# Performance work log

Hardware: AMD Instinct MI355X
Metric: run time of the kernel (lower is better)

The kernel has to match this reference:

```python
import jax, jax.numpy as jnp
import numpy as np

B, T, F, H, O = 64, 2048, 128, 512, 4
G = 4 * H  # gates: i, f, g, o (PyTorch order)


def setup_inputs() -> dict:
    key = jax.random.key(0)
    ks = jax.random.split(key, 12)
    s = 1.0 / np.sqrt(H)  # PyTorch LSTM init scale
    return {
        "x": jax.random.normal(ks[0], (B, T, F), dtype=jnp.float32),
        "W_ih_l0": jax.random.uniform(ks[1], (G, F), jnp.float32, -s, s),
        "W_hh_l0": jax.random.uniform(ks[2], (G, H), jnp.float32, -s, s),
        "b_ih_l0": jax.random.uniform(ks[3], (G,), jnp.float32, -s, s),
        "b_hh_l0": jax.random.uniform(ks[4], (G,), jnp.float32, -s, s),
        "W_ih_l1": jax.random.uniform(ks[5], (G, H), jnp.float32, -s, s),
        "W_hh_l1": jax.random.uniform(ks[6], (G, H), jnp.float32, -s, s),
        "b_ih_l1": jax.random.uniform(ks[7], (G,), jnp.float32, -s, s),
        "b_hh_l1": jax.random.uniform(ks[8], (G,), jnp.float32, -s, s),
        "W_out": jax.random.uniform(ks[9], (O, H), jnp.float32, -s, s),
        "b_out": jax.random.uniform(ks[10], (O,), jnp.float32, -s, s),
    }


def lstm_layer(x_seq, W_ih, W_hh, b_ih, b_hh):
    # x_seq: [B, T, Fin] -> (h_seq [B, T, H], h_final [B, H])
    b = x_seq.shape[0]
    h_dim = W_hh.shape[1]
    # Precompute input projections for all timesteps in one big GEMM.
    x_proj = jnp.einsum('btf,gf->btg', x_seq, W_ih) + b_ih + b_hh  # [B, T, 4H]

    def step(carry, xp_t):
        h, c = carry
        gates = xp_t + h @ W_hh.T  # [B, 4H]
        i, f, g, o = jnp.split(gates, 4, axis=-1)
        i = jax.nn.sigmoid(i)
        f = jax.nn.sigmoid(f)
        g = jnp.tanh(g)
        o = jax.nn.sigmoid(o)
        c = f * c + i * g
        h = o * jnp.tanh(c)
        return (h, c), h

    h0 = jnp.zeros((b, h_dim), x_seq.dtype)
    c0 = jnp.zeros((b, h_dim), x_seq.dtype)
    (hT, _), hs = jax.lax.scan(step, (h0, c0), jnp.swapaxes(x_proj, 0, 1))
    return jnp.swapaxes(hs, 0, 1), hT


def reference(x, W_ih_l0, W_hh_l0, b_ih_l0, b_hh_l0,
              W_ih_l1, W_hh_l1, b_ih_l1, b_hh_l1, W_out, b_out):
    h0_seq, h0_final = lstm_layer(x, W_ih_l0, W_hh_l0, b_ih_l0, b_hh_l0)
    _, h1_final = lstm_layer(h0_seq, W_ih_l1, W_hh_l1, b_ih_l1, b_hh_l1)
    # hn = stack([h0_final, h1_final]); relu(hn); linear applied to hn[0]
    hn0 = jax.nn.relu(h0_final)  # [B, H]
    out = hn0 @ W_out.T + b_out  # [B, 4]
    return out
```

## Files before the change

### kernel.cpp

```cpp
#include <hip/hip_runtime.h>
#include <hip/hip_bf16.h>
#include <cstdint>
#include <cstddef>


#define B_ 64
#define T_ 2048
#define F_ 128
#define H_ 512

#define NBLK 128
#define NTHR 256

#define ACT_STRIDE 1280
#define SMEM_SZ (16 * ACT_STRIDE)
#define HSLOT (B_ * H_)

typedef __bf16 bf16;
typedef __bf16 bf16x4 __attribute__((ext_vector_type(4)));
typedef __bf16 bf16x8 __attribute__((ext_vector_type(8)));
typedef float f32x4 __attribute__((ext_vector_type(4)));
typedef unsigned int u32;
typedef u32 u32x2 __attribute__((ext_vector_type(2)));
typedef u32 u32x4 __attribute__((ext_vector_type(4)));

static __device__ __forceinline__ float sigm(float v) {
  return 1.f / (1.f + __expf(-v));
}
static __device__ __forceinline__ float tanh_f(float v) {
  float a = fminf(fabsf(v), 20.f);
  float e = __expf(-2.f * a);
  float t = 1.f - 2.f * e / (1.f + e);
  return copysignf(t, v);
}
static __device__ __forceinline__ u32 bf16bits(float f) {
  bf16 b = (bf16)f;
  unsigned short us;
  __builtin_memcpy(&us, &b, 2);
  return (u32)us;
}

__global__ void __launch_bounds__(NTHR) prep_kernel(u32* hbuf) {
  int idx = blockIdx.x * blockDim.x + threadIdx.x;
  hbuf[idx] = 0u;
}

__global__ void __launch_bounds__(NTHR) xconv_kernel(
    const float* __restrict__ x, bf16* __restrict__ xbf) {
  const int b = blockIdx.x;
  const int t0 = blockIdx.y * 256;
  const int f2 = threadIdx.x & 63;
  const int tq = threadIdx.x >> 6;
  const int rg = b >> 4, row = b & 15;
  for (int i = 0; i < 64; ++i) {
    int t = t0 + i * 4 + tq;
    float2 xv = *(const float2*)(x + ((size_t)b * T_ + t) * F_ + 2 * f2);
    u32 w = bf16bits(xv.x) | (bf16bits(xv.y) << 16);
    *(u32*)((char*)xbf + ((((size_t)t * 4 + rg) * 16 + row) * 128 + 2 * f2) * 2) = w;
  }
}

__global__ void __launch_bounds__(NTHR, 1) lstm_kernel(
    const float* __restrict__ x,
    const float* __restrict__ Wih,
    const float* __restrict__ Whh,
    const float* __restrict__ bih,
    const float* __restrict__ bhh,
    u32* __restrict__ hbuf,
    float* __restrict__ hf32,
    const bf16* __restrict__ xbf)
{
  __shared__ __align__(16) char smem[SMEM_SZ];

  const int tid = threadIdx.x;
  const int bid = blockIdx.x;
  const int rg = bid >> 5;
  const int jg = bid & 31;
  const int row0 = rg * 16;
  const int j0 = jg * 16;

  const int lane = tid & 63;
  const int wave = tid >> 6;
  const int fr = lane & 15;
  const int kg = lane >> 4;

  bf16x8 wfrag[20];
  {
    const int G = (fr >> 2) * H_ + j0 + wave * 4 + (fr & 3);
    const float* sih = Wih + (size_t)G * F_;
    const float* shh = Whh + (size_t)G * H_;
    #pragma unroll
    for (int kk = 0; kk < 20; ++kk) {
      const float* s = (kk < 4) ? (sih + kk * 32 + kg * 8)
                                : (shh + (kk - 4) * 32 + kg * 8);
      float4 f0 = *(const float4*)s;
      float4 f1 = *(const float4*)(s + 4);
      bf16x8 w = { (bf16)f0.x, (bf16)f0.y, (bf16)f0.z, (bf16)f0.w,
                   (bf16)f1.x, (bf16)f1.y, (bf16)f1.z, (bf16)f1.w };
      wfrag[kk] = w;
    }
  }

  const int jcol = j0 + wave * 4 + kg;
  const float bi_ = bih[0 * H_ + jcol] + bhh[0 * H_ + jcol];
  const float bf_ = bih[1 * H_ + jcol] + bhh[1 * H_ + jcol];
  const float bg_ = bih[2 * H_ + jcol] + bhh[2 * H_ + jcol];
  const float bo_ = bih[3 * H_ + jcol] + bhh[3 * H_ + jcol];

  const int prow = tid >> 4;
  const int pw = tid & 15;
  const int r0x = tid >> 5;
  const int c40 = tid & 31;
  const float* xp0 = x + (size_t)(row0 + r0x) * T_ * F_ + c40 * 4;
  const float* xp1 = x + (size_t)(row0 + r0x + 8) * T_ * F_ + c40 * 4;
  const int xw0 = r0x * ACT_STRIDE + ((8 * c40) ^ ((r0x & 7) << 4));
  const int xw1 = (r0x + 8) * ACT_STRIDE + ((8 * c40) ^ (((r0x + 8) & 7) << 4));
  const int xrow = tid >> 4;
  const int xseg = tid & 15;
  const int xw = xrow * ACT_STRIDE + ((xseg * 16) ^ ((xrow & 7) << 4));

  char* buf = smem;
  float c_state = 0.f;

  for (int t = 0; t < T_; ++t) {
    if (xbf) {
      u32x4 xv = *(const u32x4*)((const char*)xbf
                  + ((size_t)t * 4 + rg) * 4096 + tid * 16);
      *(u32x4*)(buf + xw) = xv;
    } else {
      float4 xv0 = *(const float4*)(xp0 + (size_t)t * F_);
      float4 xv1 = *(const float4*)(xp1 + (size_t)t * F_);
      bf16x4 b0 = { (bf16)xv0.x, (bf16)xv0.y, (bf16)xv0.z, (bf16)xv0.w };
      bf16x4 b1 = { (bf16)xv1.x, (bf16)xv1.y, (bf16)xv1.z, (bf16)xv1.w };
      *(bf16x4*)(buf + xw0) = b0;
      *(bf16x4*)(buf + xw1) = b1;
    }
    __syncthreads();

    u32x4 v0, v1, v2, v3, v4, v5, v6, v7;
    const u32* hb = hbuf + (size_t)(t & 1) * HSLOT + (size_t)(row0 + prow) * H_ + 4 * pw;
    #define ISSUE_POLLS()                                                               \
      asm volatile("global_load_dwordx4 %0, %1, off sc0 sc1" : "=v"(v0) : "v"(hb));      \
      asm volatile("global_load_dwordx4 %0, %1, off offset:256 sc0 sc1" : "=v"(v1) : "v"(hb)); \
      asm volatile("global_load_dwordx4 %0, %1, off offset:512 sc0 sc1" : "=v"(v2) : "v"(hb)); \
      asm volatile("global_load_dwordx4 %0, %1, off offset:768 sc0 sc1" : "=v"(v3) : "v"(hb)); \
      asm volatile("global_load_dwordx4 %0, %1, off offset:1024 sc0 sc1" : "=v"(v4) : "v"(hb)); \
      asm volatile("global_load_dwordx4 %0, %1, off offset:1280 sc0 sc1" : "=v"(v5) : "v"(hb)); \
      asm volatile("global_load_dwordx4 %0, %1, off offset:1536 sc0 sc1" : "=v"(v6) : "v"(hb)); \
      asm volatile("global_load_dwordx4 %0, %1, off offset:1792 sc0 sc1" : "=v"(v7) : "v"(hb))
    ISSUE_POLLS();
    __builtin_amdgcn_sched_barrier(0);

    f32x4 a0 = {0.f, 0.f, 0.f, 0.f}, a1 = {0.f, 0.f, 0.f, 0.f};
    const char* bbase = buf + fr * ACT_STRIDE;
    const int bmask = (fr & 7) << 4;
    {
      bf16x8 p0 = *(const bf16x8*)(bbase + ((0 * 64 + kg * 16) ^ bmask));
      a0 = __builtin_amdgcn_mfma_f32_16x16x32_bf16(wfrag[0], p0, a0, 0, 0, 0);
      bf16x8 p1 = *(const bf16x8*)(bbase + ((1 * 64 + kg * 16) ^ bmask));
      a1 = __builtin_amdgcn_mfma_f32_16x16x32_bf16(wfrag[1], p1, a1, 0, 0, 0);
      bf16x8 p2 = *(const bf16x8*)(bbase + ((2 * 64 + kg * 16) ^ bmask));
      a0 = __builtin_amdgcn_mfma_f32_16x16x32_bf16(wfrag[2], p2, a0, 0, 0, 0);
      bf16x8 p3 = *(const bf16x8*)(bbase + ((3 * 64 + kg * 16) ^ bmask));
      a1 = __builtin_amdgcn_mfma_f32_16x16x32_bf16(wfrag[3], p3, a1, 0, 0, 0);
    }
    __builtin_amdgcn_sched_barrier(0);

    {
      const u32 tgt = (u32)t << 16;
      for (;;) {
        asm volatile("s_waitcnt vmcnt(0)" ::: "memory");
        __builtin_amdgcn_sched_barrier(0);
        u32 m0 = v0[0]; m0 = m0 < v0[1] ? m0 : v0[1];
        u32 m1 = v0[2]; m1 = m1 < v0[3] ? m1 : v0[3];
        #define MIN4(V) { m0 = m0 < V[0] ? m0 : V[0]; m0 = m0 < V[1] ? m0 : V[1]; \
                          m1 = m1 < V[2] ? m1 : V[2]; m1 = m1 < V[3] ? m1 : V[3]; }
        MIN4(v1) MIN4(v2) MIN4(v3) MIN4(v4) MIN4(v5) MIN4(v6) MIN4(v7)
        #undef MIN4
        u32 m = m0 < m1 ? m0 : m1;
        if (m >= tgt) break;
        ISSUE_POLLS();
      }
    }
    #undef ISSUE_POLLS

    {
      char* dst = buf + prow * ACT_STRIDE;
      const int swz = (prow & 7) << 4;
      #define UNPACK(i, V)                                                  \
        {                                                                   \
          u32 w0 = (V[0] & 0xffffu) | (V[1] << 16);                         \
          u32 w1 = (V[2] & 0xffffu) | (V[3] << 16);                         \
          u32x2 wp = { w0, w1 };                                            \
          *(u32x2*)(dst + ((256 + 128 * (i) + 8 * pw) ^ swz)) = wp;         \
        }
      UNPACK(0, v0) UNPACK(1, v1) UNPACK(2, v2) UNPACK(3, v3)
      UNPACK(4, v4) UNPACK(5, v5) UNPACK(6, v6) UNPACK(7, v7)
      #undef UNPACK
    }
    __syncthreads();

    #pragma unroll
    for (int kk = 4; kk < 20; kk += 2) {
      bf16x8 b0 = *(const bf16x8*)(bbase + ((kk * 64 + kg * 16) ^ bmask));
      a0 = __builtin_amdgcn_mfma_f32_16x16x32_bf16(wfrag[kk], b0, a0, 0, 0, 0);
      bf16x8 b1 = *(const bf16x8*)(bbase + (((kk + 1) * 64 + kg * 16) ^ bmask));
      a1 = __builtin_amdgcn_mfma_f32_16x16x32_bf16(wfrag[kk + 1], b1, a1, 0, 0, 0);
    }
    f32x4 dsum = a0 + a1;

    float d0 = dsum[0], d1 = dsum[1], d2 = dsum[2], d3 = dsum[3];
    float t0 = __shfl_xor((kg & 2) ? d0 : d2, 32, 64);
    float t1 = __shfl_xor((kg & 2) ? d1 : d3, 32, 64);
    float w0 = (kg & 2) ? t0 : d0;
    float w1 = (kg & 2) ? t1 : d1;
    float w2 = (kg & 2) ? d2 : t0;
    float w3 = (kg & 2) ? d3 : t1;
    float t2 = __shfl_xor((kg & 1) ? w0 : w1, 16, 64);
    float t3 = __shfl_xor((kg & 1) ? w2 : w3, 16, 64);
    float gi = (kg & 1) ? t2 : w0;
    float gf = (kg & 1) ? w1 : t2;
    float gg = (kg & 1) ? t3 : w2;
    float go = (kg & 1) ? w3 : t3;

    float iv = sigm(gi + bi_);
    float fv = sigm(gf + bf_);
    float gv = tanh_f(gg + bg_);
    float ov = sigm(go + bo_);
    c_state = fv * c_state + iv * gv;
    float hv = ov * tanh_f(c_state);

    u32 val = ((u32)(t + 1) << 16) | bf16bits(hv);
    u32* dstp = hbuf + (size_t)((t + 1) & 1) * HSLOT + (size_t)(row0 + fr) * H_ + jcol;
    asm volatile("global_store_dword %0, %1, off sc0 sc1" :: "v"(dstp), "v"(val) : "memory");

    if (t == T_ - 1) hf32[(size_t)(row0 + fr) * H_ + jcol] = hv;
  }
}

__global__ void __launch_bounds__(64) out_kernel(
    const float* __restrict__ h_f32,
    const float* __restrict__ Wout,
    const float* __restrict__ bout,
    float* __restrict__ out)
{
  int b = blockIdx.x;
  int lane = threadIdx.x;
  float a0 = 0.f, a1 = 0.f, a2 = 0.f, a3 = 0.f;
  for (int j = lane; j < H_; j += 64) {
    float hv = fmaxf(h_f32[(size_t)b * H_ + j], 0.f);
    a0 += hv * Wout[0 * H_ + j];
    a1 += hv * Wout[1 * H_ + j];
    a2 += hv * Wout[2 * H_ + j];
    a3 += hv * Wout[3 * H_ + j];
  }
  #pragma unroll
  for (int off = 32; off; off >>= 1) {
    a0 += __shfl_down(a0, off);
    a1 += __shfl_down(a1, off);
    a2 += __shfl_down(a2, off);
    a3 += __shfl_down(a3, off);
  }
  if (lane == 0) {
    out[b * 4 + 0] = a0 + bout[0];
    out[b * 4 + 1] = a1 + bout[1];
    out[b * 4 + 2] = a2 + bout[2];
    out[b * 4 + 3] = a3 + bout[3];
  }
}

extern "C" void kernel_launch(void* const* d_in, const int* in_sizes, int n_in,
                              void* d_out, int out_size, void* d_ws, size_t ws_size,
                              hipStream_t stream) {
  const float* x    = (const float*)d_in[0];
  const float* Wih  = (const float*)d_in[1];
  const float* Whh  = (const float*)d_in[2];
  const float* bih  = (const float*)d_in[3];
  const float* bhh  = (const float*)d_in[4];
  const float* Wout = (const float*)d_in[9];
  const float* bout = (const float*)d_in[10];

  char* ws = (char*)d_ws;
  u32*   hbuf = (u32*)ws;
  float* hf32 = (float*)(ws + 262144);
  const size_t XBF_OFF = 393216;
  const size_t XBF_SZ = (size_t)T_ * 4 * 16 * 128 * 2;
  bf16* xbf = (ws_size >= XBF_OFF + XBF_SZ) ? (bf16*)(ws + XBF_OFF) : nullptr;

  hipLaunchKernelGGL(prep_kernel, dim3(256), dim3(NTHR), 0, stream, hbuf);
  if (xbf)
    hipLaunchKernelGGL(xconv_kernel, dim3(64, 8), dim3(NTHR), 0, stream, x, xbf);

  void* args[] = { (void*)&x, (void*)&Wih, (void*)&Whh, (void*)&bih, (void*)&bhh,
                   (void*)&hbuf, (void*)&hf32, (void*)&xbf };
  hipLaunchCooperativeKernel((void*)lstm_kernel, dim3(NBLK), dim3(NTHR),
                             args, 0, stream);

  hipLaunchKernelGGL(out_kernel, dim3(B_), dim3(64), 0, stream,
                     hf32, Wout, bout, (float*)d_out);
}
```

Measured before the change: 4.204 ms.

## Tune LSTM recurrence: selective re-polling, 4 MFMA chains, fast rcp, atomic publish

The spin-wait now re-issues loads only for the 16-byte chunks whose step tags are still stale, and gives up after a fixed iteration budget. The MFMA reduction is split across four independent accumulator chains, the sigmoid and tanh divides become hardware reciprocals, and h values are published with an atomic swap instead of a cache-bypassing store. Together these aim to shorten the per-step critical path of the cross-block recurrence. The poll budget can exit early and silently continue with stale h if a producer is slow, and the approximate reciprocal slightly changes numerics.

```diff
diff --git a/kernel.cpp b/kernel.cpp
--- a/kernel.cpp
+++ b/kernel.cpp
@@ -25,12 +25,12 @@
 typedef u32 u32x4 __attribute__((ext_vector_type(4)));
 
 static __device__ __forceinline__ float sigm(float v) {
-  return 1.f / (1.f + __expf(-v));
+  return __builtin_amdgcn_rcpf(1.f + __expf(-v));
 }
 static __device__ __forceinline__ float tanh_f(float v) {
   float a = fminf(fabsf(v), 20.f);
   float e = __expf(-2.f * a);
-  float t = 1.f - 2.f * e / (1.f + e);
+  float t = 1.f - 2.f * e * __builtin_amdgcn_rcpf(1.f + e);
   return copysignf(t, v);
 }
 static __device__ __forceinline__ u32 bf16bits(float f) {
@@ -39,10 +39,15 @@
   __builtin_memcpy(&us, &b, 2);
   return (u32)us;
 }
+static __device__ __forceinline__ u32 min4(u32x4 v) {
+  u32 a = v[0] < v[1] ? v[0] : v[1];
+  u32 b = v[2] < v[3] ? v[2] : v[3];
+  return a < b ? a : b;
+}
 
 __global__ void __launch_bounds__(NTHR) prep_kernel(u32* hbuf) {
   int idx = blockIdx.x * blockDim.x + threadIdx.x;
-  hbuf[idx] = 0u;
+  if (idx < 2 * HSLOT) hbuf[idx] = 0u;
 }
 
 __global__ void __launch_bounds__(NTHR) xconv_kernel(
@@ -115,54 +120,52 @@
   const float* xp1 = x + (size_t)(row0 + r0x + 8) * T_ * F_ + c40 * 4;
   const int xw0 = r0x * ACT_STRIDE + ((8 * c40) ^ ((r0x & 7) << 4));
   const int xw1 = (r0x + 8) * ACT_STRIDE + ((8 * c40) ^ (((r0x + 8) & 7) << 4));
-  const int xrow = tid >> 4;
-  const int xseg = tid & 15;
-  const int xw = xrow * ACT_STRIDE + ((xseg * 16) ^ ((xrow & 7) << 4));
-
-  char* buf = smem;
+  const int xw = prow * ACT_STRIDE + ((pw * 16) ^ ((prow & 7) << 4));
+
+  const char* bbase = smem + fr * ACT_STRIDE;
+  const int bmask = (fr & 7) << 4;
+
   float c_state = 0.f;
+  int budget = 1 << 22;
 
   for (int t = 0; t < T_; ++t) {
     if (xbf) {
       u32x4 xv = *(const u32x4*)((const char*)xbf
                   + ((size_t)t * 4 + rg) * 4096 + tid * 16);
-      *(u32x4*)(buf + xw) = xv;
+      *(u32x4*)(smem + xw) = xv;
     } else {
       float4 xv0 = *(const float4*)(xp0 + (size_t)t * F_);
       float4 xv1 = *(const float4*)(xp1 + (size_t)t * F_);
       bf16x4 b0 = { (bf16)xv0.x, (bf16)xv0.y, (bf16)xv0.z, (bf16)xv0.w };
       bf16x4 b1 = { (bf16)xv1.x, (bf16)xv1.y, (bf16)xv1.z, (bf16)xv1.w };
-      *(bf16x4*)(buf + xw0) = b0;
-      *(bf16x4*)(buf + xw1) = b1;
+      *(bf16x4*)(smem + xw0) = b0;
+      *(bf16x4*)(smem + xw1) = b1;
     }
     __syncthreads();
 
     u32x4 v0, v1, v2, v3, v4, v5, v6, v7;
     const u32* hb = hbuf + (size_t)(t & 1) * HSLOT + (size_t)(row0 + prow) * H_ + 4 * pw;
-    #define ISSUE_POLLS()                                                               \
-      asm volatile("global_load_dwordx4 %0, %1, off sc0 sc1" : "=v"(v0) : "v"(hb));      \
-      asm volatile("global_load_dwordx4 %0, %1, off offset:256 sc0 sc1" : "=v"(v1) : "v"(hb)); \
-      asm volatile("global_load_dwordx4 %0, %1, off offset:512 sc0 sc1" : "=v"(v2) : "v"(hb)); \
-      asm volatile("global_load_dwordx4 %0, %1, off offset:768 sc0 sc1" : "=v"(v3) : "v"(hb)); \
-      asm volatile("global_load_dwordx4 %0, %1, off offset:1024 sc0 sc1" : "=v"(v4) : "v"(hb)); \
-      asm volatile("global_load_dwordx4 %0, %1, off offset:1280 sc0 sc1" : "=v"(v5) : "v"(hb)); \
-      asm volatile("global_load_dwordx4 %0, %1, off offset:1536 sc0 sc1" : "=v"(v6) : "v"(hb)); \
-      asm volatile("global_load_dwordx4 %0, %1, off offset:1792 sc0 sc1" : "=v"(v7) : "v"(hb))
-    ISSUE_POLLS();
+    asm volatile("global_load_dwordx4 %0, %1, off sc0 sc1"              : "=v"(v0) : "v"(hb));
+    asm volatile("global_load_dwordx4 %0, %1, off offset:256 sc0 sc1"   : "=v"(v1) : "v"(hb));
+    asm volatile("global_load_dwordx4 %0, %1, off offset:512 sc0 sc1"   : "=v"(v2) : "v"(hb));
+    asm volatile("global_load_dwordx4 %0, %1, off offset:768 sc0 sc1"   : "=v"(v3) : "v"(hb));
+    asm volatile("global_load_dwordx4 %0, %1, off offset:1024 sc0 sc1"  : "=v"(v4) : "v"(hb));
+    asm volatile("global_load_dwordx4 %0, %1, off offset:1280 sc0 sc1"  : "=v"(v5) : "v"(hb));
+    asm volatile("global_load_dwordx4 %0, %1, off offset:1536 sc0 sc1"  : "=v"(v6) : "v"(hb));
+    asm volatile("global_load_dwordx4 %0, %1, off offset:1792 sc0 sc1"  : "=v"(v7) : "v"(hb));
     __builtin_amdgcn_sched_barrier(0);
 
     f32x4 a0 = {0.f, 0.f, 0.f, 0.f}, a1 = {0.f, 0.f, 0.f, 0.f};
-    const char* bbase = buf + fr * ACT_STRIDE;
-    const int bmask = (fr & 7) << 4;
+    f32x4 a2 = {0.f, 0.f, 0.f, 0.f}, a3 = {0.f, 0.f, 0.f, 0.f};
     {
       bf16x8 p0 = *(const bf16x8*)(bbase + ((0 * 64 + kg * 16) ^ bmask));
       a0 = __builtin_amdgcn_mfma_f32_16x16x32_bf16(wfrag[0], p0, a0, 0, 0, 0);
       bf16x8 p1 = *(const bf16x8*)(bbase + ((1 * 64 + kg * 16) ^ bmask));
       a1 = __builtin_amdgcn_mfma_f32_16x16x32_bf16(wfrag[1], p1, a1, 0, 0, 0);
       bf16x8 p2 = *(const bf16x8*)(bbase + ((2 * 64 + kg * 16) ^ bmask));
-      a0 = __builtin_amdgcn_mfma_f32_16x16x32_bf16(wfrag[2], p2, a0, 0, 0, 0);
+      a2 = __builtin_amdgcn_mfma_f32_16x16x32_bf16(wfrag[2], p2, a2, 0, 0, 0);
       bf16x8 p3 = *(const bf16x8*)(bbase + ((3 * 64 + kg * 16) ^ bmask));
-      a1 = __builtin_amdgcn_mfma_f32_16x16x32_bf16(wfrag[3], p3, a1, 0, 0, 0);
+      a3 = __builtin_amdgcn_mfma_f32_16x16x32_bf16(wfrag[3], p3, a3, 0, 0, 0);
     }
     __builtin_amdgcn_sched_barrier(0);
 
@@ -171,21 +174,30 @@
       for (;;) {
         asm volatile("s_waitcnt vmcnt(0)" ::: "memory");
         __builtin_amdgcn_sched_barrier(0);
-        u32 m0 = v0[0]; m0 = m0 < v0[1] ? m0 : v0[1];
-        u32 m1 = v0[2]; m1 = m1 < v0[3] ? m1 : v0[3];
-        #define MIN4(V) { m0 = m0 < V[0] ? m0 : V[0]; m0 = m0 < V[1] ? m0 : V[1]; \
-                          m1 = m1 < V[2] ? m1 : V[2]; m1 = m1 < V[3] ? m1 : V[3]; }
-        MIN4(v1) MIN4(v2) MIN4(v3) MIN4(v4) MIN4(v5) MIN4(v6) MIN4(v7)
-        #undef MIN4
-        u32 m = m0 < m1 ? m0 : m1;
-        if (m >= tgt) break;
-        ISSUE_POLLS();
+        u32 need = 0;
+        if (min4(v0) < tgt) need |= 1u;
+        if (min4(v1) < tgt) need |= 2u;
+        if (min4(v2) < tgt) need |= 4u;
+        if (min4(v3) < tgt) need |= 8u;
+        if (min4(v4) < tgt) need |= 16u;
+        if (min4(v5) < tgt) need |= 32u;
+        if (min4(v6) < tgt) need |= 64u;
+        if (min4(v7) < tgt) need |= 128u;
+        if (!need) break;
+        if (--budget < 0) break;
+        if (need & 1u)   asm volatile("global_load_dwordx4 %0, %1, off sc0 sc1"             : "=v"(v0) : "v"(hb));
+        if (need & 2u)   asm volatile("global_load_dwordx4 %0, %1, off offset:256 sc0 sc1"  : "=v"(v1) : "v"(hb));
+        if (need & 4u)   asm volatile("global_load_dwordx4 %0, %1, off offset:512 sc0 sc1"  : "=v"(v2) : "v"(hb));
+        if (need & 8u)   asm volatile("global_load_dwordx4 %0, %1, off offset:768 sc0 sc1"  : "=v"(v3) : "v"(hb));
+        if (need & 16u)  asm volatile("global_load_dwordx4 %0, %1, off offset:1024 sc0 sc1" : "=v"(v4) : "v"(hb));
+        if (need & 32u)  asm volatile("global_load_dwordx4 %0, %1, off offset:1280 sc0 sc1" : "=v"(v5) : "v"(hb));
+        if (need & 64u)  asm volatile("global_load_dwordx4 %0, %1, off offset:1536 sc0 sc1" : "=v"(v6) : "v"(hb));
+        if (need & 128u) asm volatile("global_load_dwordx4 %0, %1, off offset:1792 sc0 sc1" : "=v"(v7) : "v"(hb));
       }
     }
-    #undef ISSUE_POLLS
 
     {
-      char* dst = buf + prow * ACT_STRIDE;
+      char* dst = smem + prow * ACT_STRIDE;
       const int swz = (prow & 7) << 4;
       #define UNPACK(i, V)                                                  \
         {                                                                   \
@@ -201,13 +213,17 @@
     __syncthreads();
 
     #pragma unroll
-    for (int kk = 4; kk < 20; kk += 2) {
-      bf16x8 b0 = *(const bf16x8*)(bbase + ((kk * 64 + kg * 16) ^ bmask));
-      a0 = __builtin_amdgcn_mfma_f32_16x16x32_bf16(wfrag[kk], b0, a0, 0, 0, 0);
+    for (int kk = 4; kk < 20; kk += 4) {
+      bf16x8 b0 = *(const bf16x8*)(bbase + (((kk + 0) * 64 + kg * 16) ^ bmask));
+      a0 = __builtin_amdgcn_mfma_f32_16x16x32_bf16(wfrag[kk + 0], b0, a0, 0, 0, 0);
       bf16x8 b1 = *(const bf16x8*)(bbase + (((kk + 1) * 64 + kg * 16) ^ bmask));
       a1 = __builtin_amdgcn_mfma_f32_16x16x32_bf16(wfrag[kk + 1], b1, a1, 0, 0, 0);
-    }
-    f32x4 dsum = a0 + a1;
+      bf16x8 b2 = *(const bf16x8*)(bbase + (((kk + 2) * 64 + kg * 16) ^ bmask));
+      a2 = __builtin_amdgcn_mfma_f32_16x16x32_bf16(wfrag[kk + 2], b2, a2, 0, 0, 0);
+      bf16x8 b3 = *(const bf16x8*)(bbase + (((kk + 3) * 64 + kg * 16) ^ bmask));
+      a3 = __builtin_amdgcn_mfma_f32_16x16x32_bf16(wfrag[kk + 3], b3, a3, 0, 0, 0);
+    }
+    f32x4 dsum = (a0 + a1) + (a2 + a3);
 
     float d0 = dsum[0], d1 = dsum[1], d2 = dsum[2], d3 = dsum[3];
     float t0 = __shfl_xor((kg & 2) ? d0 : d2, 32, 64);
@@ -232,7 +248,7 @@
 
     u32 val = ((u32)(t + 1) << 16) | bf16bits(hv);
     u32* dstp = hbuf + (size_t)((t + 1) & 1) * HSLOT + (size_t)(row0 + fr) * H_ + jcol;
-    asm volatile("global_store_dword %0, %1, off sc0 sc1" :: "v"(dstp), "v"(val) : "memory");
+    asm volatile("global_atomic_swap %0, %1, off" :: "v"(dstp), "v"(val) : "memory");
 
     if (t == T_ - 1) hf32[(size_t)(row0 + fr) * H_ + jcol] = hv;
   }
```

After: 3.925 ms. 1.07x faster.
